# Optimization experiments

Measured on AMD Instinct MI355X. Metric: run time of the kernel, lower is better.

Reference implementation:

```python
import jax, jax.numpy as jnp
import numpy as np

N_NODES = 50000


def _sage_conv(x, src, dst, w_l, b_l, w_r):
    """PyG SAGEConv with mean aggregation: lin_l(mean_j x_j) + lin_r(x_i)."""
    msg = x[src]  # [E, d] gather from source nodes
    agg = jax.ops.segment_sum(msg, dst, num_segments=N_NODES)  # [N, d]
    deg = jax.ops.segment_sum(jnp.ones(dst.shape, dtype=x.dtype), dst, num_segments=N_NODES)
    agg = agg / jnp.maximum(deg, 1.0)[:, None]  # mean, zero-degree safe
    return agg @ w_l + b_l + x @ w_r


def setup_inputs() -> dict:
    key = jax.random.key(0)
    ks = jax.random.split(key, 6)
    in_dim, hid, out = 128, 512, 40
    x = jax.random.normal(ks[0], (N_NODES, in_dim), dtype=jnp.float32)
    edge_index = jax.random.randint(ks[1], (2, 800000), 0, N_NODES, dtype=jnp.int64)
    s1 = 1.0 / np.sqrt(in_dim)
    s2 = 1.0 / np.sqrt(hid)
    return {
        "x": x,
        "edge_index": edge_index,
        "w1_l": jax.random.normal(ks[2], (in_dim, hid), dtype=jnp.float32) * s1,
        "b1": jnp.zeros((hid,), dtype=jnp.float32),
        "w1_r": jax.random.normal(ks[3], (in_dim, hid), dtype=jnp.float32) * s1,
        "w2_l": jax.random.normal(ks[4], (hid, out), dtype=jnp.float32) * s2,
        "b2": jnp.zeros((out,), dtype=jnp.float32),
        "w2_r": jax.random.normal(ks[5], (hid, out), dtype=jnp.float32) * s2,
    }


def reference(x, edge_index, w1_l, b1, w1_r, w2_l, b2, w2_r):
    src, dst = edge_index[0], edge_index[1]
    h = _sage_conv(x, src, dst, w1_l, b1, w1_r)
    h = jax.nn.relu(h)  # dropout is identity at inference
    h = _sage_conv(h, src, dst, w2_l, b2, w2_r)
    return jax.nn.log_softmax(h, axis=1)
```

## Files before the change

kernel.cpp:

```cpp
#include <hip/hip_runtime.h>
#include <math.h>

#define N_NODES 50000
#define N_EDGES 800000
#define IN_DIM 128
#define HID 512
#define OUT_DIM 40
#define NRANGE 8
#define RANGE_SZ ((N_NODES + NRANGE - 1) / NRANGE)
#define NCHUNK 250
#define PER_CHUNK 3200
#define CAP 64

#define FILL_BLKS (NRANGE * NCHUNK)
#define CVTX_BLKS 6250
#define CVTW_BLKS 672
#define FUSED_BLKS (FILL_BLKS + CVTX_BLKS + CVTW_BLKS)

typedef __attribute__((ext_vector_type(8))) short bf16x8;
typedef __attribute__((ext_vector_type(4))) float f32x4;
typedef __attribute__((ext_vector_type(4))) int i32x4;

__device__ __forceinline__ ushort f2bf(float f) {
    unsigned u = __float_as_uint(f);
    u += 0x7fff + ((u >> 16) & 1);
    return (ushort)(u >> 16);
}

__device__ __forceinline__ float bf2f(ushort u) {
    return __uint_as_float(((unsigned)u) << 16);
}

__device__ __forceinline__ void gload_lds16(const ushort* g, ushort* l) {
    __builtin_amdgcn_global_load_lds(
        (__attribute__((address_space(1))) void*)g,
        (__attribute__((address_space(3))) void*)l, 16, 0, 0);
}

__global__ void fill_and_prep(
    const int* __restrict__ src, const int* __restrict__ dst,
    int* __restrict__ cursor, ushort* __restrict__ csr,
    const float* __restrict__ x, ushort* __restrict__ abuf,
    const float* __restrict__ w1l, const float* __restrict__ w1r,
    const float* __restrict__ w2l, const float* __restrict__ w2r,
    ushort* __restrict__ wt, ushort* __restrict__ wt2) {
    int b = blockIdx.x, t = threadIdx.x;
    if (b < FILL_BLKS) {
        int range = b & (NRANGE - 1);
        int chunk = b >> 3;
        int lo = range * RANGE_SZ;
        int hi = lo + RANGE_SZ; if (hi > N_NODES) hi = N_NODES;
        int beg = chunk * PER_CHUNK;
        for (int e = beg + t * 4; e < beg + PER_CHUNK; e += 1024) {
            i32x4 d4 = *(const i32x4*)(dst + e);
            i32x4 s4 = *(const i32x4*)(src + e);
            if (d4.x >= lo && d4.x < hi) {
                int pos = atomicAdd(&cursor[d4.x], 1);
                if (pos < CAP) csr[d4.x * CAP + pos] = (ushort)s4.x;
            }
            if (d4.y >= lo && d4.y < hi) {
                int pos = atomicAdd(&cursor[d4.y], 1);
                if (pos < CAP) csr[d4.y * CAP + pos] = (ushort)s4.y;
            }
            if (d4.z >= lo && d4.z < hi) {
                int pos = atomicAdd(&cursor[d4.z], 1);
                if (pos < CAP) csr[d4.z * CAP + pos] = (ushort)s4.z;
            }
            if (d4.w >= lo && d4.w < hi) {
                int pos = atomicAdd(&cursor[d4.w], 1);
                if (pos < CAP) csr[d4.w * CAP + pos] = (ushort)s4.w;
            }
        }
    } else if (b < FILL_BLKS + CVTX_BLKS) {
        int i = (b - FILL_BLKS) * 256 + t;
        int n = i >> 5, qq = i & 31;
        float4 v = *(const float4*)(x + (size_t)n * 128 + qq * 4);
        ushort4 o;
        o.x = f2bf(v.x); o.y = f2bf(v.y); o.z = f2bf(v.z); o.w = f2bf(v.w);
        *(ushort4*)(abuf + (size_t)n * 256 + 128 + qq * 4) = o;
    } else {
        int i = (b - FILL_BLKS - CVTX_BLKS) * 256 + t;
        if (i < 512 * 256) {
            int k = i >> 9, c = i & 511;
            float v = (k < 128) ? w1l[(size_t)k * 512 + c] : w1r[(size_t)(k - 128) * 512 + c];
            wt[(size_t)c * 256 + k] = f2bf(v);
        } else {
            int j = i - 512 * 256;
            int c = j >> 9, k = j & 511;
            float v = (c < 40) ? w2l[(size_t)k * 40 + c] : w2r[(size_t)k * 40 + (c - 40)];
            wt2[(size_t)c * 512 + k] = f2bf(v);
        }
    }
}

__global__ void agg_x(const int* __restrict__ cursor,
                      const ushort* __restrict__ csr, ushort* __restrict__ abuf) {
    int wid = threadIdx.x >> 6;
    int lane = threadIdx.x & 63;
    int n = blockIdx.x * 4 + wid;
    if (n >= N_NODES) return;
    int d = cursor[n]; if (d > CAP) d = CAP;
    int beg = n * CAP, end = beg + d;
    int half = lane >> 5, l32 = lane & 31;
    const ushort* xb = abuf + 128;
    float a0 = 0, a1 = 0, a2 = 0, a3 = 0;
    float b0 = 0, b1 = 0, b2_ = 0, b3 = 0;
    int e = beg + half;
    for (; e + 2 < end; e += 4) {
        int s0 = csr[e], s1 = csr[e + 2];
        ushort4 v0 = *(const ushort4*)(xb + (size_t)s0 * 256 + l32 * 4);
        ushort4 v1 = *(const ushort4*)(xb + (size_t)s1 * 256 + l32 * 4);
        a0 += bf2f(v0.x); a1 += bf2f(v0.y); a2 += bf2f(v0.z); a3 += bf2f(v0.w);
        b0 += bf2f(v1.x); b1 += bf2f(v1.y); b2_ += bf2f(v1.z); b3 += bf2f(v1.w);
    }
    if (e < end) {
        int s = csr[e];
        ushort4 v = *(const ushort4*)(xb + (size_t)s * 256 + l32 * 4);
        a0 += bf2f(v.x); a1 += bf2f(v.y); a2 += bf2f(v.z); a3 += bf2f(v.w);
    }
    a0 += b0; a1 += b1; a2 += b2_; a3 += b3;
    a0 += __shfl_xor(a0, 32);
    a1 += __shfl_xor(a1, 32);
    a2 += __shfl_xor(a2, 32);
    a3 += __shfl_xor(a3, 32);
    if (d < 1) d = 1;
    float inv = 1.0f / (float)d;
    if (half == 0) {
        ushort4 o;
        o.x = f2bf(a0 * inv); o.y = f2bf(a1 * inv);
        o.z = f2bf(a2 * inv); o.w = f2bf(a3 * inv);
        *(ushort4*)(abuf + (size_t)n * 256 + l32 * 4) = o;
    }
}

#define EPI_LD 136
__global__ __launch_bounds__(256) void gemm_fused(
    const ushort* __restrict__ A, const ushort* __restrict__ WT,
    const ushort* __restrict__ WT2, const float* __restrict__ bias,
    ushort* __restrict__ p, float* __restrict__ r) {
    __shared__ ushort As[128 * 64];
    __shared__ ushort Bs[128 * 64];
    __shared__ ushort hbuf[128 * EPI_LD];
    int tid = threadIdx.x;
    int wave = tid >> 6, lane = tid & 63;
    int wm = wave >> 1, wn = wave & 1;
    int r16 = lane & 15, q = lane >> 4;
    int row0 = blockIdx.x * 128;

    f32x4 acc2[2][5] = {};

    for (int cc = 0; cc < 4; ++cc) {
        f32x4 acc1[4][4] = {};
        for (int kk = 0; kk < 256; kk += 64) {
            #pragma unroll
            for (int c = 0; c < 4; ++c) {
                int ch = wave + c * 4;
                int o = ch * 1024 + lane * 16;
                int row = o >> 7;
                int s = (o >> 4) & 7;
                int ssrc = s ^ (row & 7);
                int gr = row0 + row; if (gr > N_NODES - 1) gr = N_NODES - 1;
                gload_lds16(A + (size_t)gr * 256 + kk + (ssrc << 3), As + ch * 512);
                int gc = cc * 128 + row;
                gload_lds16(WT + (size_t)gc * 256 + kk + (ssrc << 3), Bs + ch * 512);
            }
            __syncthreads();
            #pragma unroll
            for (int kc = 0; kc < 2; ++kc) {
                int sbase = kc * 4 + q;
                bf16x8 af[4], bfr[4];
                #pragma unroll
                for (int m = 0; m < 4; ++m) {
                    int row = wm * 64 + m * 16 + r16;
                    af[m] = *(const bf16x8*)(As + row * 64 + ((sbase ^ (row & 7)) << 3));
                }
                #pragma unroll
                for (int n = 0; n < 4; ++n) {
                    int row = wn * 64 + n * 16 + r16;
                    bfr[n] = *(const bf16x8*)(Bs + row * 64 + ((sbase ^ (row & 7)) << 3));
                }
                #pragma unroll
                for (int m = 0; m < 4; ++m)
                    #pragma unroll
                    for (int n = 0; n < 4; ++n)
                        acc1[m][n] = __builtin_amdgcn_mfma_f32_16x16x32_bf16(af[m], bfr[n], acc1[m][n], 0, 0, 0);
            }
            __syncthreads();
        }

        #pragma unroll
        for (int n = 0; n < 4; ++n) {
            int col_l = wn * 64 + n * 16 + r16;
            float b = bias[cc * 128 + col_l];
            #pragma unroll
            for (int m = 0; m < 4; ++m) {
                #pragma unroll
                for (int j = 0; j < 4; ++j) {
                    int row_l = wm * 64 + m * 16 + q * 4 + j;
                    hbuf[row_l * EPI_LD + col_l] = f2bf(fmaxf(acc1[m][n][j] + b, 0.f));
                }
            }
        }
        __syncthreads();

        #pragma unroll
        for (int kw = 0; kw < 4; ++kw) {
            bf16x8 af2[2], bf2v[5];
            #pragma unroll
            for (int m = 0; m < 2; ++m) {
                int row = wave * 32 + m * 16 + r16;
                af2[m] = *(const bf16x8*)(hbuf + row * EPI_LD + kw * 32 + q * 8);
            }
            #pragma unroll
            for (int n = 0; n < 5; ++n)
                bf2v[n] = *(const bf16x8*)(WT2 + (size_t)(n * 16 + r16) * 512
                                           + cc * 128 + kw * 32 + q * 8);
            #pragma unroll
            for (int m = 0; m < 2; ++m)
                #pragma unroll
                for (int n = 0; n < 5; ++n)
                    acc2[m][n] = __builtin_amdgcn_mfma_f32_16x16x32_bf16(af2[m], bf2v[n], acc2[m][n], 0, 0, 0);
        }
        __syncthreads();
    }

    #pragma unroll
    for (int m = 0; m < 2; ++m) {
        #pragma unroll
        for (int j = 0; j < 4; ++j) {
            int grow = row0 + wave * 32 + m * 16 + q * 4 + j;
            if (grow >= N_NODES) continue;
            #pragma unroll
            for (int n = 0; n < 5; ++n) {
                int col = n * 16 + r16;
                float v = acc2[m][n][j];
                if (col < 40) p[(size_t)grow * 40 + col] = f2bf(v);
                else          r[(size_t)grow * 40 + (col - 40)] = v;
            }
        }
    }
}

__global__ void final_kernel(const ushort* __restrict__ p, const float* __restrict__ rr,
                             const float* __restrict__ b2,
                             const int* __restrict__ cursor, const ushort* __restrict__ csr,
                             float* __restrict__ out) {
    int wid = threadIdx.x >> 6;
    int lane = threadIdx.x & 63;
    int n = blockIdx.x * 4 + wid;
    if (n >= N_NODES) return;
    int d = cursor[n]; if (d > CAP) d = CAP;
    int beg = n * CAP, end = beg + d;
    float acc0 = 0.f, acc1 = 0.f, acc2 = 0.f, acc3 = 0.f;
    int e = beg;
    if (lane < OUT_DIM) {
        for (; e + 3 < end; e += 4) {
            int s0 = csr[e], s1 = csr[e + 1];
            int s2 = csr[e + 2], s3 = csr[e + 3];
            acc0 += bf2f(p[(size_t)s0 * OUT_DIM + lane]);
            acc1 += bf2f(p[(size_t)s1 * OUT_DIM + lane]);
            acc2 += bf2f(p[(size_t)s2 * OUT_DIM + lane]);
            acc3 += bf2f(p[(size_t)s3 * OUT_DIM + lane]);
        }
        for (; e < end; ++e)
            acc0 += bf2f(p[(size_t)csr[e] * OUT_DIM + lane]);
    }
    if (d < 1) d = 1;
    float inv = 1.0f / (float)d;
    float v = (lane < OUT_DIM)
                  ? ((acc0 + acc1 + acc2 + acc3) * inv + b2[lane] + rr[(size_t)n * OUT_DIM + lane])
                  : -INFINITY;
    float m = v;
    #pragma unroll
    for (int off = 32; off; off >>= 1) m = fmaxf(m, __shfl_xor(m, off));
    float ex = (lane < OUT_DIM) ? expf(v - m) : 0.f;
    float ssum = ex;
    #pragma unroll
    for (int off = 32; off; off >>= 1) ssum += __shfl_xor(ssum, off);
    if (lane < OUT_DIM) out[(size_t)n * OUT_DIM + lane] = (v - m) - logf(ssum);
}

extern "C" void kernel_launch(void* const* d_in, const int* in_sizes, int n_in,
                              void* d_out, int out_size, void* d_ws, size_t ws_size,
                              hipStream_t stream) {
    const float* x    = (const float*)d_in[0];
    const int*   edge = (const int*)d_in[1];
    const int*   srce = edge;
    const int*   dste = edge + N_EDGES;
    const float* w1l  = (const float*)d_in[2];
    const float* b1   = (const float*)d_in[3];
    const float* w1r  = (const float*)d_in[4];
    const float* w2l  = (const float*)d_in[5];
    const float* b2   = (const float*)d_in[6];
    const float* w2r  = (const float*)d_in[7];
    float* out = (float*)d_out;

    char* ws = (char*)d_ws;
    size_t off = 0;
    auto alloc = [&](size_t bytes) -> void* {
        void* ptr = ws + off;
        off = (off + bytes + 255) & ~(size_t)255;
        return ptr;
    };
    int* cursor  = (int*)alloc((size_t)N_NODES * 4);
    ushort* csr  = (ushort*)alloc((size_t)N_NODES * CAP * 2);
    ushort* abuf = (ushort*)alloc((size_t)N_NODES * 256 * 2);
    ushort* wt   = (ushort*)alloc((size_t)512 * 256 * 2);
    ushort* wt2  = (ushort*)alloc((size_t)80 * 512 * 2);
    ushort* p    = (ushort*)alloc((size_t)N_NODES * OUT_DIM * 2);
    float* rbuf  = (float*)alloc((size_t)N_NODES * OUT_DIM * 4);

    hipMemsetAsync(cursor, 0, (size_t)N_NODES * 4, stream);
    fill_and_prep<<<FUSED_BLKS, 256, 0, stream>>>(srce, dste, cursor, csr,
                                                  x, abuf, w1l, w1r, w2l, w2r, wt, wt2);
    agg_x<<<(N_NODES + 3) / 4, 256, 0, stream>>>(cursor, csr, abuf);
    gemm_fused<<<(N_NODES + 127) / 128, 256, 0, stream>>>(abuf, wt, wt2, b1, p, rbuf);
    final_kernel<<<(N_NODES + 3) / 4, 256, 0, stream>>>(p, rbuf, b2, cursor, csr, out);
}
```

Baseline: 165.6 us.

## Halve fused GEMM row tile, alias LDS buffers, swizzle hidden tile

The fused two-layer GEMM now handles 64 rows per block instead of 128, which doubles the grid to about 782 blocks and halves the accumulator registers per wave. The hidden-activation tile shares LDS with the A/B staging tiles and uses an XOR swizzle instead of padding, so LDS use falls from roughly 67KB to 24KB per block. The aim is higher occupancy and better load balance across CUs. In exchange, each B (weight) tile loaded into LDS is reused across fewer rows, so weight traffic per output row doubles.

```diff
diff --git a/kernel.cpp b/kernel.cpp
--- a/kernel.cpp
+++ b/kernel.cpp
@@ -133,27 +133,27 @@
     }
 }
 
-#define EPI_LD 136
 __global__ __launch_bounds__(256) void gemm_fused(
     const ushort* __restrict__ A, const ushort* __restrict__ WT,
     const ushort* __restrict__ WT2, const float* __restrict__ bias,
     ushort* __restrict__ p, float* __restrict__ r) {
-    __shared__ ushort As[128 * 64];
-    __shared__ ushort Bs[128 * 64];
-    __shared__ ushort hbuf[128 * EPI_LD];
+    __shared__ ushort pool[12288];
+    ushort* As = pool;
+    ushort* Bs = pool + 4096;
+    ushort* hbuf = pool;
     int tid = threadIdx.x;
     int wave = tid >> 6, lane = tid & 63;
     int wm = wave >> 1, wn = wave & 1;
     int r16 = lane & 15, q = lane >> 4;
-    int row0 = blockIdx.x * 128;
-
-    f32x4 acc2[2][5] = {};
+    int row0 = blockIdx.x * 64;
+
+    f32x4 acc2[5] = {};
 
     for (int cc = 0; cc < 4; ++cc) {
-        f32x4 acc1[4][4] = {};
+        f32x4 acc1[2][4] = {};
         for (int kk = 0; kk < 256; kk += 64) {
             #pragma unroll
-            for (int c = 0; c < 4; ++c) {
+            for (int c = 0; c < 2; ++c) {
                 int ch = wave + c * 4;
                 int o = ch * 1024 + lane * 16;
                 int row = o >> 7;
@@ -161,6 +161,14 @@
                 int ssrc = s ^ (row & 7);
                 int gr = row0 + row; if (gr > N_NODES - 1) gr = N_NODES - 1;
                 gload_lds16(A + (size_t)gr * 256 + kk + (ssrc << 3), As + ch * 512);
+            }
+            #pragma unroll
+            for (int c = 0; c < 4; ++c) {
+                int ch = wave + c * 4;
+                int o = ch * 1024 + lane * 16;
+                int row = o >> 7;
+                int s = (o >> 4) & 7;
+                int ssrc = s ^ (row & 7);
                 int gc = cc * 128 + row;
                 gload_lds16(WT + (size_t)gc * 256 + kk + (ssrc << 3), Bs + ch * 512);
             }
@@ -168,10 +176,10 @@
             #pragma unroll
             for (int kc = 0; kc < 2; ++kc) {
                 int sbase = kc * 4 + q;
-                bf16x8 af[4], bfr[4];
+                bf16x8 af[2], bfr[4];
                 #pragma unroll
-                for (int m = 0; m < 4; ++m) {
-                    int row = wm * 64 + m * 16 + r16;
+                for (int m = 0; m < 2; ++m) {
+                    int row = wm * 32 + m * 16 + r16;
                     af[m] = *(const bf16x8*)(As + row * 64 + ((sbase ^ (row & 7)) << 3));
                 }
                 #pragma unroll
@@ -180,7 +188,7 @@
                     bfr[n] = *(const bf16x8*)(Bs + row * 64 + ((sbase ^ (row & 7)) << 3));
                 }
                 #pragma unroll
-                for (int m = 0; m < 4; ++m)
+                for (int m = 0; m < 2; ++m)
                     #pragma unroll
                     for (int n = 0; n < 4; ++n)
                         acc1[m][n] = __builtin_amdgcn_mfma_f32_16x16x32_bf16(af[m], bfr[n], acc1[m][n], 0, 0, 0);
@@ -192,51 +200,46 @@
         for (int n = 0; n < 4; ++n) {
             int col_l = wn * 64 + n * 16 + r16;
             float b = bias[cc * 128 + col_l];
-            #pragma unroll
-            for (int m = 0; m < 4; ++m) {
+            int chi = col_l >> 3, clo = col_l & 7;
+            #pragma unroll
+            for (int m = 0; m < 2; ++m) {
                 #pragma unroll
                 for (int j = 0; j < 4; ++j) {
-                    int row_l = wm * 64 + m * 16 + q * 4 + j;
-                    hbuf[row_l * EPI_LD + col_l] = f2bf(fmaxf(acc1[m][n][j] + b, 0.f));
+                    int row_l = wm * 32 + m * 16 + q * 4 + j;
+                    hbuf[row_l * 128 + (((chi ^ (row_l & 7)) << 3) | clo)] =
+                        f2bf(fmaxf(acc1[m][j == 0 ? n : n][j] + b, 0.f));
                 }
             }
         }
         __syncthreads();
 
+        int prow = wave * 16 + r16;
         #pragma unroll
         for (int kw = 0; kw < 4; ++kw) {
-            bf16x8 af2[2], bf2v[5];
-            #pragma unroll
-            for (int m = 0; m < 2; ++m) {
-                int row = wave * 32 + m * 16 + r16;
-                af2[m] = *(const bf16x8*)(hbuf + row * EPI_LD + kw * 32 + q * 8);
-            }
+            int slot = kw * 4 + q;
+            bf16x8 af2 = *(const bf16x8*)(hbuf + prow * 128 + ((slot ^ (prow & 7)) << 3));
+            bf16x8 bv[5];
             #pragma unroll
             for (int n = 0; n < 5; ++n)
-                bf2v[n] = *(const bf16x8*)(WT2 + (size_t)(n * 16 + r16) * 512
-                                           + cc * 128 + kw * 32 + q * 8);
-            #pragma unroll
-            for (int m = 0; m < 2; ++m)
-                #pragma unroll
-                for (int n = 0; n < 5; ++n)
-                    acc2[m][n] = __builtin_amdgcn_mfma_f32_16x16x32_bf16(af2[m], bf2v[n], acc2[m][n], 0, 0, 0);
+                bv[n] = *(const bf16x8*)(WT2 + (size_t)(n * 16 + r16) * 512
+                                         + cc * 128 + kw * 32 + q * 8);
+            #pragma unroll
+            for (int n = 0; n < 5; ++n)
+                acc2[n] = __builtin_amdgcn_mfma_f32_16x16x32_bf16(af2, bv[n], acc2[n], 0, 0, 0);
         }
         __syncthreads();
     }
 
     #pragma unroll
-    for (int m = 0; m < 2; ++m) {
+    for (int j = 0; j < 4; ++j) {
+        int grow = row0 + wave * 16 + q * 4 + j;
+        if (grow >= N_NODES) continue;
         #pragma unroll
-        for (int j = 0; j < 4; ++j) {
-            int grow = row0 + wave * 32 + m * 16 + q * 4 + j;
-            if (grow >= N_NODES) continue;
-            #pragma unroll
-            for (int n = 0; n < 5; ++n) {
-                int col = n * 16 + r16;
-                float v = acc2[m][n][j];
-                if (col < 40) p[(size_t)grow * 40 + col] = f2bf(v);
-                else          r[(size_t)grow * 40 + (col - 40)] = v;
-            }
+        for (int n = 0; n < 5; ++n) {
+            int col = n * 16 + r16;
+            float v = acc2[n][j];
+            if (col < 40) p[(size_t)grow * 40 + col] = f2bf(v);
+            else          r[(size_t)grow * 40 + (col - 40)] = v;
         }
     }
 }
@@ -314,6 +317,6 @@
     fill_and_prep<<<FUSED_BLKS, 256, 0, stream>>>(srce, dste, cursor, csr,
                                                   x, abuf, w1l, w1r, w2l, w2r, wt, wt2);
     agg_x<<<(N_NODES + 3) / 4, 256, 0, stream>>>(cursor, csr, abuf);
-    gemm_fused<<<(N_NODES + 127) / 128, 256, 0, stream>>>(abuf, wt, wt2, b1, p, rbuf);
+    gemm_fused<<<(N_NODES + 63) / 64, 256, 0, stream>>>(abuf, wt, wt2, b1, p, rbuf);
     final_kernel<<<(N_NODES + 3) / 4, 256, 0, stream>>>(p, rbuf, b2, cursor, csr, out);
 }
```

Measured after the change: 189.7 us. +14.5%, slower.
